# Kernel tuning notes

Hardware: AMD Instinct MI355X
Metric: run time of the kernel (lower is better)

The kernel has to match this reference:

```python
import jax, jax.numpy as jnp
import numpy as np

# Dims matching init_kwargs
B, S, D = 2, 2048, 1024
H, E, P, K = 8, 8, 128, 2
SCALE = 1.0 / np.sqrt(P)  # registered buffer 'scale'


def setup_inputs() -> dict:
    key = jax.random.key(0)
    ks = jax.random.split(key, 8)
    std = 1.0 / np.sqrt(D)  # reset_parameters uses std_scale/sqrt(input_size)
    return {
        "x": jax.random.normal(ks[0], (B, S, D), jnp.float32),
        "q_w": jax.random.normal(ks[1], (H * P, D), jnp.float32) * std,
        "k_w": jax.random.normal(ks[2], (H * P, D), jnp.float32) * std,
        "v_w": jax.random.normal(ks[3], (H * E, D, P), jnp.float32) * std,
        "o_w": jax.random.normal(ks[4], (H * E, P, D), jnp.float32) * (1.0 / np.sqrt(H * P)),
        "sel_v_w": jax.random.normal(ks[5], (H * E, D), jnp.float32) * std,
        "sel_o_w": jax.random.normal(ks[6], (H * E, D), jnp.float32) * std,
        "route_scale": jnp.ones((1,), jnp.float32),
    }


def _get_sel_gate(x, w, route_scale):
    """Faithful port of SwitchHeadCore.get_sel (eval mode, no bias):
    sigmoid routing logits per head, top-k expert selection, weight
    normalization, route_scale. Returned as a dense [B,S,H,E] gate so the
    indexed expert combine is expressed as a gated einsum (same math)."""
    logits = jnp.einsum('bsd,ed->bse', x, w).astype(jnp.float32)
    raw = logits.reshape(x.shape[0], x.shape[1], H, E)
    probs = jax.nn.sigmoid(raw)
    vals, idx = jax.lax.top_k(probs, K)                 # [B,S,H,K]
    vals = vals / jnp.clip(vals.sum(-1, keepdims=True), 1e-9)  # normalize_weights
    vals = vals * route_scale
    gate = (jax.nn.one_hot(idx, E, dtype=vals.dtype) * vals[..., None]).sum(-2)
    return gate  # [B,S,H,E]


def reference(x, q_w, k_w, v_w, o_w, sel_v_w, sel_o_w, route_scale):
    rs = route_scale[0]
    gate_v = _get_sel_gate(x, sel_v_w, rs)  # [B,S,H,E]
    gate_o = _get_sel_gate(x, sel_o_w, rs)  # [B,S,H,E]

    # q/k projections -> torch head order [B,H,S,P]
    q = jnp.einsum('bsd,hpd->bhsp', x, q_w.reshape(H, P, D))
    k = jnp.einsum('bsd,hpd->bhsp', x, k_w.reshape(H, P, D))

    # Per-token expert V projection: mixture of selected expert weight slices
    xv = jnp.einsum('bsd,hedp->bshep', x, v_w.reshape(H, E, D, P))
    v = jnp.einsum('bshep,bshe->bhsp', xv, gate_v)

    # Scaled dot-product attention (eval: no dropout)
    att = jax.nn.softmax(jnp.einsum('bhqp,bhkp->bhqk', q, k) * SCALE, axis=-1)
    ctx = jnp.einsum('bhqk,bhkp->bqhp', att, v)  # [B,S,H,P]

    # Per-token expert O projection, gated, summed over heads
    weighted = ctx[:, :, :, None, :] * gate_o[..., None]  # [B,S,H,E,P]
    out = jnp.einsum('bshep,hepd->bsd', weighted, o_w.reshape(H, E, P, D))
    return out
```

## Files before the change

kernel.cpp:

```cpp
#include <hip/hip_runtime.h>


typedef unsigned short u16;
typedef __attribute__((ext_vector_type(8))) short s8v;
typedef __attribute__((ext_vector_type(4))) float f4v;
typedef __attribute__((ext_vector_type(4))) unsigned short us4;

#define ATT_SCALE 0.08838834764831845f

__device__ inline u16 bf16_rne(float f) {
  union { float f; unsigned u; } v; v.f = f;
  unsigned r = v.u + 0x7fffu + ((v.u >> 16) & 1u);
  return (u16)(r >> 16);
}
__device__ inline float bf2f(u16 h) {
  union { unsigned u; float f; } v; v.u = ((unsigned)h) << 16;
  return v.f;
}

__device__ inline void glds16(const void* g, void* l) {
  __builtin_amdgcn_global_load_lds((const __attribute__((address_space(1))) void*)g,
                                   (__attribute__((address_space(3))) void*)l, 16, 0, 0);
}

__global__ void conv_qk(const float* __restrict__ Q, const float* __restrict__ K,
                        u16* __restrict__ Qb, u16* __restrict__ Kb) {
  int i = blockIdx.x * 256 + threadIdx.x;
  const float* src; u16* dst; int off;
  if (i < 262144) { src = Q; dst = Qb; off = i; }
  else            { src = K; dst = Kb; off = i - 262144; }
  float4 v = *(const float4*)&src[(size_t)off * 4];
  us4 o; o[0]=bf16_rne(v.x); o[1]=bf16_rne(v.y); o[2]=bf16_rne(v.z); o[3]=bf16_rne(v.w);
  *(us4*)&dst[(size_t)off * 4] = o;
}

__global__ void transpose_w(const float* __restrict__ src, u16* __restrict__ dst, int mode) {
  __shared__ float tile[32][33];
  int he = blockIdx.z;
  int C = mode ? 1024 : 128;
  int r0 = blockIdx.y * 32, c0 = blockIdx.x * 32;
  int lc = threadIdx.x & 31, rr = threadIdx.x >> 5;
  const float* s = src + (size_t)he * 131072;
#pragma unroll
  for (int i = 0; i < 4; ++i) {
    int r = rr + i * 8;
    tile[r][lc] = s[(size_t)(r0 + r) * C + c0 + lc];
  }
  __syncthreads();
#pragma unroll
  for (int i = 0; i < 4; ++i) {
    int c = rr + i * 8;
    float v = tile[lc][c];
    size_t a;
    if (mode) a = (size_t)(c0 + c) * 8192 + (size_t)he * 128 + (r0 + lc);
    else      a = (size_t)(he >> 3) * 1048576 + (size_t)(c0 + c) * 8192 + (size_t)(he & 7) * 1024 + (r0 + lc);
    dst[a] = bf16_rne(v);
  }
}

__global__ __launch_bounds__(256, 2) void routing(
    const float* __restrict__ X, const float* __restrict__ SelV, const float* __restrict__ SelO,
    const float* __restrict__ RS, int2* __restrict__ Tvi, float2* __restrict__ Tvg,
    int2* __restrict__ Toi, float2* __restrict__ Tog, u16* __restrict__ Xb) {
  __shared__ float xs[8][1024];
  __shared__ float lgs[8][128];
  int t0 = blockIdx.x * 8;
  int tid = threadIdx.x;
  for (int i = tid; i < 2048; i += 256) {
    int row = i >> 8, c = (i & 255) * 4;
    float4 v = *(const float4*)&X[(size_t)(t0 + row) * 1024 + c];
    *(float4*)&xs[row][c] = v;
    us4 o; o[0]=bf16_rne(v.x); o[1]=bf16_rne(v.y); o[2]=bf16_rne(v.z); o[3]=bf16_rne(v.w);
    *(us4*)&Xb[(size_t)(t0 + row) * 1024 + c] = o;
  }
  __syncthreads();
  {
    int widx = tid & 127, tg = tid >> 7;
    const float* w = (widx < 64) ? (SelV + (size_t)widx * 1024) : (SelO + (size_t)(widx - 64) * 1024);
    float acc[4] = {0.f, 0.f, 0.f, 0.f};
    for (int k = 0; k < 1024; k += 4) {
      float4 wv = *(const float4*)&w[k];
#pragma unroll
      for (int t = 0; t < 4; ++t) {
        float4 xv = *(const float4*)&xs[tg * 4 + t][k];
        acc[t] += wv.x * xv.x + wv.y * xv.y + wv.z * xv.z + wv.w * xv.w;
      }
    }
#pragma unroll
    for (int t = 0; t < 4; ++t) lgs[tg * 4 + t][widx] = acc[t];
  }
  __syncthreads();
  if (tid < 128) {
    float rs = RS[0];
    int tok = tid >> 4, which = (tid >> 3) & 1, h = tid & 7;
    float p[8];
#pragma unroll
    for (int e = 0; e < 8; ++e)
      p[e] = 1.f / (1.f + __expf(-lgs[tok][which * 64 + h * 8 + e]));
    float v1 = -1.f; int i1 = -1;
#pragma unroll
    for (int e = 0; e < 8; ++e) if (p[e] > v1) { v1 = p[e]; i1 = e; }
    float v2 = -1.f; int i2 = -1;
#pragma unroll
    for (int e = 0; e < 8; ++e) if (e != i1 && p[e] > v2) { v2 = p[e]; i2 = e; }
    float ssum = fmaxf(v1 + v2, 1e-9f);
    float g1 = v1 / ssum * rs, g2 = v2 / ssum * rs;
    int t = t0 + tok;
    int lo, hi; float glo, ghi;
    if (i1 < i2) { lo = i1; hi = i2; glo = g1; ghi = g2; }
    else         { lo = i2; hi = i1; glo = g2; ghi = g1; }
    if (which) { Toi[t * 8 + h] = make_int2(lo, hi); Tog[t * 8 + h] = make_float2(glo, ghi); }
    else       { Tvi[t * 8 + h] = make_int2(lo, hi); Tvg[t * 8 + h] = make_float2(glo, ghi); }
  }
}

__global__ void build_buckets(const int2* __restrict__ Tvi, const float2* __restrict__ Tvg,
                              int* __restrict__ bcnt, u16* __restrict__ btok,
                              float2* __restrict__ bgate) {
  int t = blockIdx.x * 256 + threadIdx.x;
#pragma unroll
  for (int h = 0; h < 8; ++h) {
    int2 e = Tvi[t * 8 + h];
    int pid = e.x * 7 - (e.x * (e.x - 1)) / 2 + (e.y - e.x - 1);
    int b = h * 28 + pid;
    int pos = atomicAdd(&bcnt[b], 1);
    if (pos < 1024) { btok[b * 1024 + pos] = (u16)t; bgate[b * 1024 + pos] = Tvg[t * 8 + h]; }
  }
}

__global__ __launch_bounds__(256) void gemm_qk(
    const u16* __restrict__ Xb, const u16* __restrict__ Wq, const u16* __restrict__ Wk,
    u16* __restrict__ Qo, u16* __restrict__ Ko) {
  __shared__ u16 Ash[128 * 32];
  __shared__ u16 Bsh[128 * 32];
  const int tb = blockIdx.x, nb = blockIdx.y;
  const u16* W = blockIdx.z ? Wk : Wq;
  u16* Out = blockIdx.z ? Ko : Qo;
  const int tid = threadIdx.x;
  const int wave = tid >> 6, lane = tid & 63;
  const int wm = wave >> 1, wn = wave & 1;
  const int lg = lane >> 4, lr = lane & 15;
  f4v acc[4][4] = {};
  for (int kt = 0; kt < 32; ++kt) {
    __syncthreads();
#pragma unroll
    for (int i = 0; i < 2; ++i) {
      int idx = tid + i * 256;
      int r = idx >> 2, c8 = (idx & 3) << 3;
      glds16(&Xb[(size_t)(tb * 128 + r) * 1024 + kt * 32 + c8], &Ash[idx * 8]);
      glds16(&W[(size_t)(nb * 128 + r) * 1024 + kt * 32 + c8], &Bsh[idx * 8]);
    }
    __syncthreads();
    s8v af[4], bfr[4];
#pragma unroll
    for (int m = 0; m < 4; ++m) af[m] = *(const s8v*)&Ash[(wm * 64 + m * 16 + lr) * 32 + lg * 8];
#pragma unroll
    for (int n = 0; n < 4; ++n) bfr[n] = *(const s8v*)&Bsh[(wn * 64 + n * 16 + lr) * 32 + lg * 8];
#pragma unroll
    for (int m = 0; m < 4; ++m)
#pragma unroll
      for (int n = 0; n < 4; ++n)
        acc[m][n] = __builtin_amdgcn_mfma_f32_16x16x32_bf16(af[m], bfr[n], acc[m][n], 0, 0, 0);
  }
#pragma unroll
  for (int m = 0; m < 4; ++m) {
    int tbase = tb * 128 + wm * 64 + m * 16 + lg * 4;
    int b = tbase >> 11, s = tbase & 2047;
#pragma unroll
    for (int n = 0; n < 4; ++n) {
      int p = wn * 64 + n * 16 + lr;
      size_t base = ((size_t)(b * 8 + nb) * 2048 + s) * 128 + p;
#pragma unroll
      for (int j = 0; j < 4; ++j)
        Out[base + (size_t)j * 128] = bf16_rne(acc[m][n][j]);
    }
  }
}

__global__ __launch_bounds__(256, 4) void gemm_v_sparse(
    const u16* __restrict__ Xb, const u16* __restrict__ Vw ,
    const int* __restrict__ bcnt, const u16* __restrict__ btok,
    const float2* __restrict__ bgate, u16* __restrict__ Vtmp) {
  const int bucket = blockIdx.y;
  const int h = bucket / 28, pid = bucket % 28;
  const int cnt = min(bcnt[bucket], 512);
  const int tile = blockIdx.x;
  if (tile * 64 >= cnt) return;
  int lo = 0, rem = pid;
  while (rem >= 7 - lo) { rem -= 7 - lo; lo++; }
  const int hi = lo + 1 + rem;
  __shared__ u16 Ash[64 * 32];
  __shared__ u16 BshL[128 * 32];
  __shared__ u16 BshH[128 * 32];
  __shared__ int toksh[64];
  __shared__ float g0sh[64], g1sh[64];
  const int tid = threadIdx.x;
  if (tid < 64) {
    int ar = tile * 64 + tid;
    if (ar < cnt) {
      toksh[tid] = btok[bucket * 1024 + ar];
      float2 g = bgate[bucket * 1024 + ar];
      g0sh[tid] = g.x; g1sh[tid] = g.y;
    } else { toksh[tid] = 0; g0sh[tid] = 0.f; g1sh[tid] = 0.f; }
  }
  __syncthreads();
  const int wave = tid >> 6, lane = tid & 63;
  const int lg = lane >> 4, lr = lane & 15;
  const int rA = tid >> 2, cA = (tid & 3) << 3;
  const int tokA = toksh[rA];
  const int rB0 = tid >> 2, cB0 = (tid & 3) << 3;
  const int rB1 = (tid + 256) >> 2, cB1 = cB0;
  const size_t bwL0 = ((size_t)(h * 128 + rB0) * 8 + lo) * 1024 + cB0;
  const size_t bwL1 = ((size_t)(h * 128 + rB1) * 8 + lo) * 1024 + cB1;
  const size_t bwH0 = ((size_t)(h * 128 + rB0) * 8 + hi) * 1024 + cB0;
  const size_t bwH1 = ((size_t)(h * 128 + rB1) * 8 + hi) * 1024 + cB1;
  const size_t aw = (size_t)tokA * 1024 + cA;
  f4v accL[4][2] = {};
  f4v accH[4][2] = {};
  for (int kt = 0; kt < 32; ++kt) {
    const int d0 = kt * 32;
    __syncthreads();
    glds16(&Xb[aw + d0], &Ash[tid * 8]);
    glds16(&Vw[bwL0 + d0], &BshL[tid * 8]);
    glds16(&Vw[bwL1 + d0], &BshL[(tid + 256) * 8]);
    glds16(&Vw[bwH0 + d0], &BshH[tid * 8]);
    glds16(&Vw[bwH1 + d0], &BshH[(tid + 256) * 8]);
    __syncthreads();
    s8v af[4], bl[2], bh[2];
#pragma unroll
    for (int m = 0; m < 4; ++m) af[m] = *(const s8v*)&Ash[(m * 16 + lr) * 32 + lg * 8];
#pragma unroll
    for (int n = 0; n < 2; ++n) {
      bl[n] = *(const s8v*)&BshL[(wave * 32 + n * 16 + lr) * 32 + lg * 8];
      bh[n] = *(const s8v*)&BshH[(wave * 32 + n * 16 + lr) * 32 + lg * 8];
    }
#pragma unroll
    for (int m = 0; m < 4; ++m)
#pragma unroll
      for (int n = 0; n < 2; ++n) {
        accL[m][n] = __builtin_amdgcn_mfma_f32_16x16x32_bf16(af[m], bl[n], accL[m][n], 0, 0, 0);
        accH[m][n] = __builtin_amdgcn_mfma_f32_16x16x32_bf16(af[m], bh[n], accH[m][n], 0, 0, 0);
      }
  }
#pragma unroll
  for (int m = 0; m < 4; ++m) {
#pragma unroll
    for (int j = 0; j < 4; ++j) {
      int row = m * 16 + lg * 4 + j;
      int ar = tile * 64 + row;
      if (ar < cnt) {
        int tok = toksh[row];
        float g0 = g0sh[row], g1 = g1sh[row];
#pragma unroll
        for (int n = 0; n < 2; ++n) {
          int p = wave * 32 + n * 16 + lr;
          Vtmp[(size_t)tok * 1024 + h * 128 + p] = bf16_rne(g0 * accL[m][n][j] + g1 * accH[m][n][j]);
        }
      }
    }
  }
}

__global__ void vtranspose(const u16* __restrict__ Vtmp, u16* __restrict__ VT) {
  __shared__ u16 tile[64][136];
  const int sb = blockIdx.x, bh = blockIdx.y;
  const int b = bh >> 3, h = bh & 7;
  const int tid = threadIdx.x;
#pragma unroll
  for (int it = 0; it < 4; ++it) {
    int idx = tid + it * 256;
    int r = idx >> 4, c8 = (idx & 15) << 3;
    *(s8v*)&tile[r][c8] = *(const s8v*)&Vtmp[(size_t)(b * 2048 + sb * 64 + r) * 1024 + h * 128 + c8];
  }
  __syncthreads();
#pragma unroll
  for (int it = 0; it < 8; ++it) {
    int idx = tid + it * 256;
    int p = idx >> 4, c4 = (idx & 15) << 2;
    us4 o;
#pragma unroll
    for (int j = 0; j < 4; ++j) o[j] = tile[c4 + j][p];
    *(us4*)&VT[((size_t)bh * 128 + p) * 2048 + sb * 64 + c4] = o;
  }
}

__global__ __launch_bounds__(256, 2) void attn(
    const u16* __restrict__ Q, const u16* __restrict__ K,
    const u16* __restrict__ VT, u16* __restrict__ CTX) {
  __shared__ u16 Kt[64 * 136];
  __shared__ u16 Vt[128 * 72];
  __shared__ u16 Pl[4][16 * 72];
  const int qb = blockIdx.x, bh = blockIdx.y;
  const int tid = threadIdx.x;
  const int wave = tid >> 6, lane = tid & 63;
  const int lg = lane >> 4, lr = lane & 15;
  const size_t base = (size_t)bh * 2048 * 128;
  const int q0 = qb * 64 + wave * 16;
  s8v qf[4];
#pragma unroll
  for (int ks = 0; ks < 4; ++ks)
    qf[ks] = *(const s8v*)&Q[base + (size_t)(q0 + lr) * 128 + ks * 32 + lg * 8];
  f4v cacc[8] = {};
  float mrun = -1e30f, ssum = 0.f;
  for (int kb = 0; kb < 32; ++kb) {
    __syncthreads();
#pragma unroll
    for (int i = 0; i < 4; ++i) {
      int idx = tid + i * 256;
      int r = idx >> 4, c8 = (idx & 15) << 3;
      *(s8v*)&Kt[r * 136 + c8] = *(const s8v*)&K[base + (size_t)(kb * 64 + r) * 128 + c8];
    }
#pragma unroll
    for (int i = 0; i < 4; ++i) {
      int idx = tid + i * 256;
      int r = idx >> 3, c8 = (idx & 7) << 3;
      *(s8v*)&Vt[r * 72 + c8] = *(const s8v*)&VT[base + (size_t)r * 2048 + kb * 64 + c8];
    }
    __syncthreads();
    f4v sc[4] = {};
#pragma unroll
    for (int ks = 0; ks < 4; ++ks) {
#pragma unroll
      for (int m = 0; m < 4; ++m) {
        s8v ak = *(const s8v*)&Kt[(m * 16 + lr) * 136 + ks * 32 + lg * 8];
        sc[m] = __builtin_amdgcn_mfma_f32_16x16x32_bf16(ak, qf[ks], sc[m], 0, 0, 0);
      }
    }
    float tmax = -1e30f;
#pragma unroll
    for (int m = 0; m < 4; ++m)
#pragma unroll
      for (int j = 0; j < 4; ++j) {
        float v = sc[m][j] * ATT_SCALE;
        sc[m][j] = v;
        tmax = fmaxf(tmax, v);
      }
    tmax = fmaxf(tmax, __shfl_xor(tmax, 16));
    tmax = fmaxf(tmax, __shfl_xor(tmax, 32));
    float mnew = fmaxf(mrun, tmax);
    float f = __expf(mrun - mnew);
    mrun = mnew;
    float psum = 0.f;
#pragma unroll
    for (int m = 0; m < 4; ++m) {
      us4 pk;
#pragma unroll
      for (int j = 0; j < 4; ++j) {
        float pe = __expf(sc[m][j] - mnew);
        psum += pe;
        pk[j] = bf16_rne(pe);
      }
      *(us4*)&Pl[wave][lr * 72 + m * 16 + lg * 4] = pk;
    }
    psum += __shfl_xor(psum, 16);
    psum += __shfl_xor(psum, 32);
    ssum = ssum * f + psum;
#pragma unroll
    for (int mr = 0; mr < 8; ++mr)
#pragma unroll
      for (int j = 0; j < 4; ++j) cacc[mr][j] *= f;
#pragma unroll
    for (int ks = 0; ks < 2; ++ks) {
      s8v bp = *(const s8v*)&Pl[wave][lr * 72 + ks * 32 + lg * 8];
#pragma unroll
      for (int mr = 0; mr < 8; ++mr) {
        s8v av = *(const s8v*)&Vt[(mr * 16 + lr) * 72 + ks * 32 + lg * 8];
        cacc[mr] = __builtin_amdgcn_mfma_f32_16x16x32_bf16(av, bp, cacc[mr], 0, 0, 0);
      }
    }
  }
  float rinv = 1.f / ssum;
#pragma unroll
  for (int mr = 0; mr < 8; ++mr) {
    us4 pk;
#pragma unroll
    for (int j = 0; j < 4; ++j) pk[j] = bf16_rne(cacc[mr][j] * rinv);
    *(us4*)&CTX[base + (size_t)(q0 + lr) * 128 + mr * 16 + lg * 4] = pk;
  }
}

__global__ __launch_bounds__(256) void pregate(
    const u16* __restrict__ CTX, const int2* __restrict__ Toi, const float2* __restrict__ Tog,
    u16* __restrict__ CTXG) {
  const int t = blockIdx.x;
  const int tid = threadIdx.x;
  __shared__ float gsh[64];
  if (tid < 64) {
    int h = tid >> 3, e = tid & 7;
    int2 ei = Toi[t * 8 + h];
    float2 gg = Tog[t * 8 + h];
    gsh[tid] = (e == ei.x) ? gg.x : ((e == ei.y) ? gg.y : 0.f);
  }
  __syncthreads();
  const int b = t >> 11, s = t & 2047;
#pragma unroll
  for (int c = 0; c < 4; ++c) {
    int chunk = tid + c * 256;
    int he = chunk >> 4, p8 = (chunk & 15) << 3;
    int h = he >> 3;
    float g = gsh[he];
    s8v o;
    if (g != 0.f) {
      s8v v = *(const s8v*)&CTX[((size_t)(b * 8 + h) * 2048 + s) * 128 + p8];
#pragma unroll
      for (int j = 0; j < 8; ++j) o[j] = (short)bf16_rne(bf2f((u16)v[j]) * g);
    } else {
#pragma unroll
      for (int j = 0; j < 8; ++j) o[j] = 0;
    }
    *(s8v*)&CTXG[(size_t)t * 8192 + chunk * 8] = o;
  }
}

__global__ __launch_bounds__(256) void gemm_o_dense(
    const u16* __restrict__ CTXG, const u16* __restrict__ Ow ,
    float* __restrict__ OUT, float* __restrict__ OP1a, float* __restrict__ OP1b) {
  __shared__ u16 Ash[128 * 32];
  __shared__ u16 Bsh[128 * 32];
  const int tb = blockIdx.x, db = blockIdx.y, kz = blockIdx.z;
  const int tid = threadIdx.x;
  const int wave = tid >> 6, lane = tid & 63;
  const int wm = wave >> 1, wn = wave & 1;
  const int lg = lane >> 4, lr = lane & 15;
  const size_t kbase = (size_t)kz * 4096;
  f4v acc[4][4] = {};
  for (int kt = 0; kt < 128; ++kt) {
    __syncthreads();
#pragma unroll
    for (int i = 0; i < 2; ++i) {
      int idx = tid + i * 256;
      int r = idx >> 2, c8 = (idx & 3) << 3;
      glds16(&CTXG[(size_t)(tb * 128 + r) * 8192 + kbase + kt * 32 + c8], &Ash[idx * 8]);
      glds16(&Ow[(size_t)(db * 128 + r) * 8192 + kbase + kt * 32 + c8], &Bsh[idx * 8]);
    }
    __syncthreads();
    s8v af[4], bfr[4];
#pragma unroll
    for (int m = 0; m < 4; ++m) af[m] = *(const s8v*)&Ash[(wm * 64 + m * 16 + lr) * 32 + lg * 8];
#pragma unroll
    for (int n = 0; n < 4; ++n) bfr[n] = *(const s8v*)&Bsh[(wn * 64 + n * 16 + lr) * 32 + lg * 8];
#pragma unroll
    for (int m = 0; m < 4; ++m)
#pragma unroll
      for (int n = 0; n < 4; ++n)
        acc[m][n] = __builtin_amdgcn_mfma_f32_16x16x32_bf16(af[m], bfr[n], acc[m][n], 0, 0, 0);
  }
  float* OP;
  if (kz == 0) OP = OUT;
  else OP = (tb < 16) ? OP1a : OP1b;
  const int toff = (kz == 0) ? tb * 128 : (tb & 15) * 128;
#pragma unroll
  for (int m = 0; m < 4; ++m) {
    int t = toff + wm * 64 + m * 16 + lg * 4;
#pragma unroll
    for (int n = 0; n < 4; ++n) {
      int d = db * 128 + wn * 64 + n * 16 + lr;
#pragma unroll
      for (int j = 0; j < 4; ++j)
        OP[(size_t)(t + j) * 1024 + d] = acc[m][n][j];
    }
  }
}

__global__ void add_inplace(float* __restrict__ OUT, const float* __restrict__ P0,
                            const float* __restrict__ P1) {
  size_t i = ((size_t)blockIdx.x * 256 + threadIdx.x) * 4;
  const float* P = (i < 2097152) ? (P0 + i) : (P1 + (i - 2097152));
  float4 a = *(const float4*)&OUT[i];
  float4 b = *(const float4*)P;
  *(float4*)&OUT[i] = make_float4(a.x + b.x, a.y + b.y, a.z + b.z, a.w + b.w);
}

extern "C" void kernel_launch(void* const* d_in, const int* in_sizes, int n_in,
                              void* d_out, int out_size, void* d_ws, size_t ws_size,
                              hipStream_t stream) {
  const float* x     = (const float*)d_in[0];
  const float* q_w   = (const float*)d_in[1];
  const float* k_w   = (const float*)d_in[2];
  const float* v_w   = (const float*)d_in[3];
  const float* o_w   = (const float*)d_in[4];
  const float* sel_v = (const float*)d_in[5];
  const float* sel_o = (const float*)d_in[6];
  const float* rs    = (const float*)d_in[7];

  char* ws = (char*)d_ws;
  const size_t MB = 1048576;
  const size_t KB = 1024;
  u16*    xb    = (u16*)(ws);
  u16*    ctx   = (u16*)(ws);
  float*  op1a  = (float*)(ws);
  u16*    qwb   = (u16*)(ws + 8 * MB);
  u16*    kwb   = (u16*)(ws + 10 * MB);
  u16*    ctxg  = (u16*)(ws + 8 * MB);
  u16*    vwT   = (u16*)(ws + 12 * MB);
  u16*    vt    = (u16*)(ws + 12 * MB);
  u16*    vtmp  = (u16*)(ws + 49 * MB + 512 * KB);
  u16*    qh    = (u16*)(ws + 49 * MB + 512 * KB);
  u16*    kh    = (u16*)(ws + 57 * MB + 512 * KB);
  int2*   tvi   = (int2*)(ws + 72 * MB);
  float2* tvg   = (float2*)(ws + 72 * MB + 256 * KB);
  int2*   toi   = (int2*)(ws + 72 * MB + 512 * KB);
  float2* tog   = (float2*)(ws + 72 * MB + 768 * KB);
  int*    bcntv = (int*)(ws + 73 * MB);
  u16*    btokv = (u16*)(ws + 73 * MB + 8 * KB);
  float2* bgatev= (float2*)(ws + 73 * MB + 512 * KB);
  float*  op1b  = (float*)(ws + 72 * MB);
  u16*    owT   = (u16*)(ws + 80 * MB);
  float*  outp  = (float*)d_out;

  hipLaunchKernelGGL(conv_qk, dim3(2048), dim3(256), 0, stream, q_w, k_w, qwb, kwb);
  hipLaunchKernelGGL(transpose_w, dim3(4, 32, 64), dim3(256), 0, stream, v_w, vwT, 0);
  hipLaunchKernelGGL(transpose_w, dim3(32, 4, 64), dim3(256), 0, stream, o_w, owT, 1);
  hipMemsetAsync(bcntv, 0, 4 * KB, stream);
  hipLaunchKernelGGL(routing, dim3(512), dim3(256), 0, stream, x, sel_v, sel_o, rs, tvi, tvg, toi, tog, xb);
  hipLaunchKernelGGL(build_buckets, dim3(16), dim3(256), 0, stream, tvi, tvg, bcntv, btokv, bgatev);
  hipLaunchKernelGGL(gemm_v_sparse, dim3(8, 224), dim3(256), 0, stream, xb, vwT, bcntv, btokv, bgatev, vtmp);
  hipLaunchKernelGGL(vtranspose, dim3(32, 16), dim3(256), 0, stream, vtmp, vt);
  hipLaunchKernelGGL(gemm_qk, dim3(32, 8, 2), dim3(256), 0, stream, xb, qwb, kwb, qh, kh);
  hipLaunchKernelGGL(attn, dim3(32, 16), dim3(256), 0, stream, qh, kh, vt, ctx);
  hipLaunchKernelGGL(pregate, dim3(4096), dim3(256), 0, stream, ctx, toi, tog, ctxg);
  hipLaunchKernelGGL(gemm_o_dense, dim3(32, 8, 2), dim3(256), 0, stream, ctxg, owT, outp, op1a, op1b);
  hipLaunchKernelGGL(add_inplace, dim3(4096), dim3(256), 0, stream, outp, op1a, op1b);
}
```

Measured before the change: 439.6 us.

## Double-buffer LDS tiles with XOR swizzle in QK, V and O GEMMs

Adds ping-pong LDS buffers to the three MFMA GEMM kernels, so the next K-slice's global-to-LDS loads are issued while the current slice is computed. Column chunks are XOR-swizzled by row to reduce LDS bank conflicts on fragment reads. The QK GEMM tile shrinks from 128 to 64 rows and the grid doubles to give more blocks. The V GEMM drops its occupancy hint. Doubling LDS per block may lower occupancy, and a full vmcnt(0) wait at every step limits how much the loads can overlap.

```diff
diff --git a/kernel.cpp b/kernel.cpp
--- a/kernel.cpp
+++ b/kernel.cpp
@@ -22,6 +22,11 @@
   __builtin_amdgcn_global_load_lds((const __attribute__((address_space(1))) void*)g,
                                    (__attribute__((address_space(3))) void*)l, 16, 0, 0);
 }
+__device__ inline int swzcol(int idx) {
+  int r = idx >> 2;
+  return (((idx & 3) ^ ((r + (r >> 2)) & 3)) << 3);
+}
+#define WAITB() do { asm volatile("s_waitcnt vmcnt(0)" ::: "memory"); __syncthreads(); } while (0)
 
 __global__ void conv_qk(const float* __restrict__ Q, const float* __restrict__ K,
                         u16* __restrict__ Qb, u16* __restrict__ Kb) {
@@ -131,44 +136,52 @@
 __global__ __launch_bounds__(256) void gemm_qk(
     const u16* __restrict__ Xb, const u16* __restrict__ Wq, const u16* __restrict__ Wk,
     u16* __restrict__ Qo, u16* __restrict__ Ko) {
-  __shared__ u16 Ash[128 * 32];
-  __shared__ u16 Bsh[128 * 32];
+  __shared__ u16 Ash0[64 * 32], Ash1[64 * 32];
+  __shared__ u16 Bsh0[128 * 32], Bsh1[128 * 32];
   const int tb = blockIdx.x, nb = blockIdx.y;
   const u16* W = blockIdx.z ? Wk : Wq;
   u16* Out = blockIdx.z ? Ko : Qo;
   const int tid = threadIdx.x;
   const int wave = tid >> 6, lane = tid & 63;
-  const int wm = wave >> 1, wn = wave & 1;
   const int lg = lane >> 4, lr = lane & 15;
-  f4v acc[4][4] = {};
-  for (int kt = 0; kt < 32; ++kt) {
-    __syncthreads();
-#pragma unroll
-    for (int i = 0; i < 2; ++i) {
-      int idx = tid + i * 256;
-      int r = idx >> 2, c8 = (idx & 3) << 3;
-      glds16(&Xb[(size_t)(tb * 128 + r) * 1024 + kt * 32 + c8], &Ash[idx * 8]);
-      glds16(&W[(size_t)(nb * 128 + r) * 1024 + kt * 32 + c8], &Bsh[idx * 8]);
-    }
-    __syncthreads();
-    s8v af[4], bfr[4];
-#pragma unroll
-    for (int m = 0; m < 4; ++m) af[m] = *(const s8v*)&Ash[(wm * 64 + m * 16 + lr) * 32 + lg * 8];
-#pragma unroll
-    for (int n = 0; n < 4; ++n) bfr[n] = *(const s8v*)&Bsh[(wn * 64 + n * 16 + lr) * 32 + lg * 8];
-#pragma unroll
-    for (int m = 0; m < 4; ++m)
-#pragma unroll
-      for (int n = 0; n < 4; ++n)
-        acc[m][n] = __builtin_amdgcn_mfma_f32_16x16x32_bf16(af[m], bfr[n], acc[m][n], 0, 0, 0);
-  }
+  const int r0 = tid >> 2, r1 = (tid + 256) >> 2;
+  const int c0 = swzcol(tid), c1 = swzcol(tid + 256);
+  const size_t aw  = (size_t)(tb * 64 + r0) * 1024 + c0;
+  const size_t bw0 = (size_t)(nb * 128 + r0) * 1024 + c0;
+  const size_t bw1 = (size_t)(nb * 128 + r1) * 1024 + c1;
+  const int csl = (lg ^ ((lr + (lr >> 2)) & 3)) << 3;
+  f4v acc[4][2] = {};
+#define STG_QK(A, B, k0) do { \
+    glds16(&Xb[aw + (k0)], &A[tid * 8]); \
+    glds16(&W[bw0 + (k0)], &B[tid * 8]); \
+    glds16(&W[bw1 + (k0)], &B[(tid + 256) * 8]); \
+  } while (0)
+#define CMP_QK(A, B) do { \
+    s8v af[4], bfr[2]; \
+    _Pragma("unroll") for (int m = 0; m < 4; ++m) af[m] = *(const s8v*)&A[(m * 16 + lr) * 32 + csl]; \
+    _Pragma("unroll") for (int n = 0; n < 2; ++n) bfr[n] = *(const s8v*)&B[(wave * 32 + n * 16 + lr) * 32 + csl]; \
+    _Pragma("unroll") for (int m = 0; m < 4; ++m) \
+      _Pragma("unroll") for (int n = 0; n < 2; ++n) \
+        acc[m][n] = __builtin_amdgcn_mfma_f32_16x16x32_bf16(af[m], bfr[n], acc[m][n], 0, 0, 0); \
+  } while (0)
+  STG_QK(Ash0, Bsh0, 0);
+  for (int kt = 0; kt < 32; kt += 2) {
+    WAITB();
+    if (kt + 1 < 32) STG_QK(Ash1, Bsh1, (kt + 1) * 32);
+    CMP_QK(Ash0, Bsh0);
+    WAITB();
+    if (kt + 2 < 32) STG_QK(Ash0, Bsh0, (kt + 2) * 32);
+    CMP_QK(Ash1, Bsh1);
+  }
+#undef STG_QK
+#undef CMP_QK
 #pragma unroll
   for (int m = 0; m < 4; ++m) {
-    int tbase = tb * 128 + wm * 64 + m * 16 + lg * 4;
+    int tbase = tb * 64 + m * 16 + lg * 4;
     int b = tbase >> 11, s = tbase & 2047;
 #pragma unroll
-    for (int n = 0; n < 4; ++n) {
-      int p = wn * 64 + n * 16 + lr;
+    for (int n = 0; n < 2; ++n) {
+      int p = wave * 32 + n * 16 + lr;
       size_t base = ((size_t)(b * 8 + nb) * 2048 + s) * 128 + p;
 #pragma unroll
       for (int j = 0; j < 4; ++j)
@@ -177,7 +190,7 @@
   }
 }
 
-__global__ __launch_bounds__(256, 4) void gemm_v_sparse(
+__global__ __launch_bounds__(256) void gemm_v_sparse(
     const u16* __restrict__ Xb, const u16* __restrict__ Vw ,
     const int* __restrict__ bcnt, const u16* __restrict__ btok,
     const float2* __restrict__ bgate, u16* __restrict__ Vtmp) {
@@ -189,9 +202,9 @@
   int lo = 0, rem = pid;
   while (rem >= 7 - lo) { rem -= 7 - lo; lo++; }
   const int hi = lo + 1 + rem;
-  __shared__ u16 Ash[64 * 32];
-  __shared__ u16 BshL[128 * 32];
-  __shared__ u16 BshH[128 * 32];
+  __shared__ u16 Ash0[64 * 32], Ash1[64 * 32];
+  __shared__ u16 BL0[128 * 32], BL1[128 * 32];
+  __shared__ u16 BH0[128 * 32], BH1[128 * 32];
   __shared__ int toksh[64];
   __shared__ float g0sh[64], g1sh[64];
   const int tid = threadIdx.x;
@@ -206,42 +219,48 @@
   __syncthreads();
   const int wave = tid >> 6, lane = tid & 63;
   const int lg = lane >> 4, lr = lane & 15;
-  const int rA = tid >> 2, cA = (tid & 3) << 3;
-  const int tokA = toksh[rA];
-  const int rB0 = tid >> 2, cB0 = (tid & 3) << 3;
-  const int rB1 = (tid + 256) >> 2, cB1 = cB0;
-  const size_t bwL0 = ((size_t)(h * 128 + rB0) * 8 + lo) * 1024 + cB0;
-  const size_t bwL1 = ((size_t)(h * 128 + rB1) * 8 + lo) * 1024 + cB1;
-  const size_t bwH0 = ((size_t)(h * 128 + rB0) * 8 + hi) * 1024 + cB0;
-  const size_t bwH1 = ((size_t)(h * 128 + rB1) * 8 + hi) * 1024 + cB1;
-  const size_t aw = (size_t)tokA * 1024 + cA;
+  const int r0 = tid >> 2, r1 = (tid + 256) >> 2;
+  const int c0 = swzcol(tid), c1 = swzcol(tid + 256);
+  const int tokA = toksh[r0];
+  const size_t aw   = (size_t)tokA * 1024 + c0;
+  const size_t bwL0 = ((size_t)(h * 128 + r0) * 8 + lo) * 1024 + c0;
+  const size_t bwL1 = ((size_t)(h * 128 + r1) * 8 + lo) * 1024 + c1;
+  const size_t bwH0 = ((size_t)(h * 128 + r0) * 8 + hi) * 1024 + c0;
+  const size_t bwH1 = ((size_t)(h * 128 + r1) * 8 + hi) * 1024 + c1;
+  const int csl = (lg ^ ((lr + (lr >> 2)) & 3)) << 3;
   f4v accL[4][2] = {};
   f4v accH[4][2] = {};
-  for (int kt = 0; kt < 32; ++kt) {
-    const int d0 = kt * 32;
-    __syncthreads();
-    glds16(&Xb[aw + d0], &Ash[tid * 8]);
-    glds16(&Vw[bwL0 + d0], &BshL[tid * 8]);
-    glds16(&Vw[bwL1 + d0], &BshL[(tid + 256) * 8]);
-    glds16(&Vw[bwH0 + d0], &BshH[tid * 8]);
-    glds16(&Vw[bwH1 + d0], &BshH[(tid + 256) * 8]);
-    __syncthreads();
-    s8v af[4], bl[2], bh[2];
-#pragma unroll
-    for (int m = 0; m < 4; ++m) af[m] = *(const s8v*)&Ash[(m * 16 + lr) * 32 + lg * 8];
-#pragma unroll
-    for (int n = 0; n < 2; ++n) {
-      bl[n] = *(const s8v*)&BshL[(wave * 32 + n * 16 + lr) * 32 + lg * 8];
-      bh[n] = *(const s8v*)&BshH[(wave * 32 + n * 16 + lr) * 32 + lg * 8];
-    }
-#pragma unroll
-    for (int m = 0; m < 4; ++m)
-#pragma unroll
-      for (int n = 0; n < 2; ++n) {
-        accL[m][n] = __builtin_amdgcn_mfma_f32_16x16x32_bf16(af[m], bl[n], accL[m][n], 0, 0, 0);
-        accH[m][n] = __builtin_amdgcn_mfma_f32_16x16x32_bf16(af[m], bh[n], accH[m][n], 0, 0, 0);
-      }
-  }
+#define STG_V(A, BL, BH, d0) do { \
+    glds16(&Xb[aw + (d0)], &A[tid * 8]); \
+    glds16(&Vw[bwL0 + (d0)], &BL[tid * 8]); \
+    glds16(&Vw[bwL1 + (d0)], &BL[(tid + 256) * 8]); \
+    glds16(&Vw[bwH0 + (d0)], &BH[tid * 8]); \
+    glds16(&Vw[bwH1 + (d0)], &BH[(tid + 256) * 8]); \
+  } while (0)
+#define CMP_V(A, BL, BH) do { \
+    s8v af[4], bl[2], bh[2]; \
+    _Pragma("unroll") for (int m = 0; m < 4; ++m) af[m] = *(const s8v*)&A[(m * 16 + lr) * 32 + csl]; \
+    _Pragma("unroll") for (int n = 0; n < 2; ++n) { \
+      bl[n] = *(const s8v*)&BL[(wave * 32 + n * 16 + lr) * 32 + csl]; \
+      bh[n] = *(const s8v*)&BH[(wave * 32 + n * 16 + lr) * 32 + csl]; \
+    } \
+    _Pragma("unroll") for (int m = 0; m < 4; ++m) \
+      _Pragma("unroll") for (int n = 0; n < 2; ++n) { \
+        accL[m][n] = __builtin_amdgcn_mfma_f32_16x16x32_bf16(af[m], bl[n], accL[m][n], 0, 0, 0); \
+        accH[m][n] = __builtin_amdgcn_mfma_f32_16x16x32_bf16(af[m], bh[n], accH[m][n], 0, 0, 0); \
+      } \
+  } while (0)
+  STG_V(Ash0, BL0, BH0, 0);
+  for (int kt = 0; kt < 32; kt += 2) {
+    WAITB();
+    if (kt + 1 < 32) STG_V(Ash1, BL1, BH1, (kt + 1) * 32);
+    CMP_V(Ash0, BL0, BH0);
+    WAITB();
+    if (kt + 2 < 32) STG_V(Ash0, BL0, BH0, (kt + 2) * 32);
+    CMP_V(Ash1, BL1, BH1);
+  }
+#undef STG_V
+#undef CMP_V
 #pragma unroll
   for (int m = 0; m < 4; ++m) {
 #pragma unroll
@@ -415,36 +434,47 @@
 __global__ __launch_bounds__(256) void gemm_o_dense(
     const u16* __restrict__ CTXG, const u16* __restrict__ Ow ,
     float* __restrict__ OUT, float* __restrict__ OP1a, float* __restrict__ OP1b) {
-  __shared__ u16 Ash[128 * 32];
-  __shared__ u16 Bsh[128 * 32];
+  __shared__ u16 Ash0[128 * 32], Ash1[128 * 32];
+  __shared__ u16 Bsh0[128 * 32], Bsh1[128 * 32];
   const int tb = blockIdx.x, db = blockIdx.y, kz = blockIdx.z;
   const int tid = threadIdx.x;
   const int wave = tid >> 6, lane = tid & 63;
   const int wm = wave >> 1, wn = wave & 1;
   const int lg = lane >> 4, lr = lane & 15;
   const size_t kbase = (size_t)kz * 4096;
+  const int r0 = tid >> 2, r1 = (tid + 256) >> 2;
+  const int c0 = swzcol(tid), c1 = swzcol(tid + 256);
+  const size_t aw0 = (size_t)(tb * 128 + r0) * 8192 + kbase + c0;
+  const size_t aw1 = (size_t)(tb * 128 + r1) * 8192 + kbase + c1;
+  const size_t bw0 = (size_t)(db * 128 + r0) * 8192 + kbase + c0;
+  const size_t bw1 = (size_t)(db * 128 + r1) * 8192 + kbase + c1;
+  const int csl = (lg ^ ((lr + (lr >> 2)) & 3)) << 3;
   f4v acc[4][4] = {};
-  for (int kt = 0; kt < 128; ++kt) {
-    __syncthreads();
-#pragma unroll
-    for (int i = 0; i < 2; ++i) {
-      int idx = tid + i * 256;
-      int r = idx >> 2, c8 = (idx & 3) << 3;
-      glds16(&CTXG[(size_t)(tb * 128 + r) * 8192 + kbase + kt * 32 + c8], &Ash[idx * 8]);
-      glds16(&Ow[(size_t)(db * 128 + r) * 8192 + kbase + kt * 32 + c8], &Bsh[idx * 8]);
-    }
-    __syncthreads();
-    s8v af[4], bfr[4];
-#pragma unroll
-    for (int m = 0; m < 4; ++m) af[m] = *(const s8v*)&Ash[(wm * 64 + m * 16 + lr) * 32 + lg * 8];
-#pragma unroll
-    for (int n = 0; n < 4; ++n) bfr[n] = *(const s8v*)&Bsh[(wn * 64 + n * 16 + lr) * 32 + lg * 8];
-#pragma unroll
-    for (int m = 0; m < 4; ++m)
-#pragma unroll
-      for (int n = 0; n < 4; ++n)
-        acc[m][n] = __builtin_amdgcn_mfma_f32_16x16x32_bf16(af[m], bfr[n], acc[m][n], 0, 0, 0);
-  }
+#define STG_O(A, B, k0) do { \
+    glds16(&CTXG[aw0 + (k0)], &A[tid * 8]); \
+    glds16(&CTXG[aw1 + (k0)], &A[(tid + 256) * 8]); \
+    glds16(&Ow[bw0 + (k0)], &B[tid * 8]); \
+    glds16(&Ow[bw1 + (k0)], &B[(tid + 256) * 8]); \
+  } while (0)
+#define CMP_O(A, B) do { \
+    s8v af[4], bfr[4]; \
+    _Pragma("unroll") for (int m = 0; m < 4; ++m) af[m] = *(const s8v*)&A[(wm * 64 + m * 16 + lr) * 32 + csl]; \
+    _Pragma("unroll") for (int n = 0; n < 4; ++n) bfr[n] = *(const s8v*)&B[(wn * 64 + n * 16 + lr) * 32 + csl]; \
+    _Pragma("unroll") for (int m = 0; m < 4; ++m) \
+      _Pragma("unroll") for (int n = 0; n < 4; ++n) \
+        acc[m][n] = __builtin_amdgcn_mfma_f32_16x16x32_bf16(af[m], bfr[n], acc[m][n], 0, 0, 0); \
+  } while (0)
+  STG_O(Ash0, Bsh0, 0);
+  for (int kt = 0; kt < 128; kt += 2) {
+    WAITB();
+    if (kt + 1 < 128) STG_O(Ash1, Bsh1, (kt + 1) * 32);
+    CMP_O(Ash0, Bsh0);
+    WAITB();
+    if (kt + 2 < 128) STG_O(Ash0, Bsh0, (kt + 2) * 32);
+    CMP_O(Ash1, Bsh1);
+  }
+#undef STG_O
+#undef CMP_O
   float* OP;
   if (kz == 0) OP = OUT;
   else OP = (tb < 16) ? OP1a : OP1b;
@@ -516,7 +546,7 @@
   hipLaunchKernelGGL(build_buckets, dim3(16), dim3(256), 0, stream, tvi, tvg, bcntv, btokv, bgatev);
   hipLaunchKernelGGL(gemm_v_sparse, dim3(8, 224), dim3(256), 0, stream, xb, vwT, bcntv, btokv, bgatev, vtmp);
   hipLaunchKernelGGL(vtranspose, dim3(32, 16), dim3(256), 0, stream, vtmp, vt);
-  hipLaunchKernelGGL(gemm_qk, dim3(32, 8, 2), dim3(256), 0, stream, xb, qwb, kwb, qh, kh);
+  hipLaunchKernelGGL(gemm_qk, dim3(64, 8, 2), dim3(256), 0, stream, xb, qwb, kwb, qh, kh);
   hipLaunchKernelGGL(attn, dim3(32, 16), dim3(256), 0, stream, qh, kh, vt, ctx);
   hipLaunchKernelGGL(pregate, dim3(4096), dim3(256), 0, stream, ctx, toi, tog, ctxg);
   hipLaunchKernelGGL(gemm_o_dense, dim3(32, 8, 2), dim3(256), 0, stream, ctxg, owT, outp, op1a, op1b);
```

After: 424.3 us. 3.5% less time.
